# Kernel optimization log

Hardware: AMD Instinct MI355X
Metric: run time of the kernel (lower is better)

Reference implementation:

```python
import jax, jax.numpy as jnp
import numpy as np

# Coefficients expressing each of the 16 soft binary logic gates as
# c0 + ca*a + cb*b + cab*(a*b), in standard difflogic op order:
# 0:False 1:AND 2:a&~b 3:A 4:~a&b 5:B 6:XOR 7:OR 8:NOR 9:XNOR
# 10:~B 11:B=>A 12:~A 13:A=>B 14:NAND 15:True
GATE_COEF = jnp.array([
    [0, 0, 0, 0],
    [0, 0, 0, 1],
    [0, 1, 0, -1],
    [0, 1, 0, 0],
    [0, 0, 1, -1],
    [0, 0, 1, 0],
    [0, 1, 1, -2],
    [0, 1, 1, -1],
    [1, -1, -1, 1],
    [1, -1, -1, 2],
    [1, 0, -1, 0],
    [1, 0, -1, 1],
    [1, -1, 0, 0],
    [1, -1, 0, 1],
    [1, 0, 0, -1],
    [1, 0, 0, 0],
], dtype=jnp.float32)  # [16, 4]

INPUT_DIM = 8192
HIDDEN_DIMS = [16384, 16384, 16384, 16384]
OUTPUT_DIM = 1000
BATCH = 2048
TAU = 1.0
N_GATES = 16


def setup_inputs() -> dict:
    key = jax.random.key(0)
    kx, key = jax.random.split(key)
    inp = {"x": jax.random.uniform(kx, (BATCH, INPUT_DIM), dtype=jnp.float32)}
    dims = [INPUT_DIM] + HIDDEN_DIMS + [OUTPUT_DIM]
    for i in range(len(dims) - 1):
        in_d, out_d = dims[i], dims[i + 1]
        kw, ka, kb, key = jax.random.split(key, 4)
        inp[f"w{i}"] = jax.random.normal(kw, (out_d, N_GATES), dtype=jnp.float32)
        inp[f"ia{i}"] = jax.random.randint(ka, (out_d,), 0, in_d, dtype=jnp.int32)
        inp[f"ib{i}"] = jax.random.randint(kb, (out_d,), 0, in_d, dtype=jnp.int32)
    return inp


def _logic_layer(x, w, ia, ib):
    # gather the two inputs of every neuron: [batch, out_dim]
    a = x[:, ia]
    b = x[:, ib]
    p = jax.nn.softmax(w, axis=-1)              # [out_dim, 16]
    coef = p @ GATE_COEF                         # [out_dim, 4]
    # weighted mixture of all 16 gates, fused via bilinear form
    return coef[:, 0] + coef[:, 1] * a + coef[:, 2] * b + coef[:, 3] * (a * b)


def reference(x, w0, w1, w2, w3, w4, ia0, ia1, ia2, ia3, ia4, ib0, ib1, ib2, ib3, ib4):
    ws = [w0, w1, w2, w3, w4]
    ias = [ia0, ia1, ia2, ia3, ia4]
    ibs = [ib0, ib1, ib2, ib3, ib4]
    h = x
    for w, ia, ib in zip(ws, ias, ibs):
        h = _logic_layer(h, w, ia, ib)
    # GroupSum(output_dim, tau): split last dim into output_dim groups, sum, /tau
    batch = h.shape[0]
    group = h.shape[-1] // OUTPUT_DIM
    out = h.reshape(batch, OUTPUT_DIM, group).sum(-1) / TAU
    return out
```

## Files before the change

kernel.cpp:

```cpp
#include <hip/hip_runtime.h>


#define NBATCH 2048
#define IN_DIM 8192
#define HID 16384
#define OUT_DIM 1000
#define NTOT (4 * HID + OUT_DIM)

typedef __attribute__((ext_vector_type(4))) _Float16 half4;

__device__ __constant__ float GC_dev[64] = {
    0, 0, 0, 0,   0, 0, 0, 1,   0, 1, 0, -1,  0, 1, 0, 0,
    0, 0, 1, -1,  0, 0, 1, 0,   0, 1, 1, -2,  0, 1, 1, -1,
    1, -1, -1, 1, 1, -1, -1, 2, 1, 0, -1, 0,  1, 0, -1, 1,
    1, -1, 0, 0,  1, -1, 0, 1,  1, 0, 0, -1,  1, 0, 0, 0
};

struct PrepArgs {
    const float* w[5];
    const int* ia[5];
    const int* ib[5];
};

__global__ __launch_bounds__(256) void prep_kernel(
    PrepArgs args, half4* __restrict__ coefT, unsigned int* __restrict__ idxT) {
    int g = blockIdx.x * 256 + threadIdx.x;
    if (g >= NTOT) return;
    int l = (g < 4 * HID) ? (g >> 14) : 4;
    int j = g - l * HID;

    const float* wrow = args.w[l] + (size_t)j * 16;
    float v[16];
    const float4* w4 = (const float4*)wrow;
#pragma unroll
    for (int i = 0; i < 4; ++i) {
        float4 t = w4[i];
        v[4 * i + 0] = t.x; v[4 * i + 1] = t.y; v[4 * i + 2] = t.z; v[4 * i + 3] = t.w;
    }
    float m = v[0];
#pragma unroll
    for (int g2 = 1; g2 < 16; ++g2) m = fmaxf(m, v[g2]);
    float s = 0.f;
#pragma unroll
    for (int g2 = 0; g2 < 16; ++g2) { v[g2] = __expf(v[g2] - m); s += v[g2]; }
    float inv = 1.f / s;
    float c0 = 0.f, c1 = 0.f, c2 = 0.f, c3 = 0.f;
#pragma unroll
    for (int g2 = 0; g2 < 16; ++g2) {
        c0 += v[g2] * GC_dev[g2 * 4 + 0];
        c1 += v[g2] * GC_dev[g2 * 4 + 1];
        c2 += v[g2] * GC_dev[g2 * 4 + 2];
        c3 += v[g2] * GC_dev[g2 * 4 + 3];
    }
    half4 c;
    c[0] = (_Float16)(c0 * inv); c[1] = (_Float16)(c1 * inv);
    c[2] = (_Float16)(c2 * inv); c[3] = (_Float16)(c3 * inv);
    coefT[g] = c;
    idxT[g] = (unsigned int)args.ia[l][j] | ((unsigned int)args.ib[l][j] << 16);
}

__global__ __launch_bounds__(512) void fused_kernel(
    const float* __restrict__ x, const half4* __restrict__ coefT,
    const unsigned int* __restrict__ idxT, float* __restrict__ out) {
    __shared__ _Float16 lds[2 * HID];
    int b = blockIdx.x;
    int t = threadIdx.x;

    const float4* xr = (const float4*)(x + (size_t)b * IN_DIM);
#pragma unroll
    for (int i = 0; i < 4; ++i) {
        int j = i * 2048 + t * 4;
        float4 v = xr[i * 512 + t];
        half4 h;
        h[0] = (_Float16)v.x; h[1] = (_Float16)v.y;
        h[2] = (_Float16)v.z; h[3] = (_Float16)v.w;
        *(half4*)&lds[j] = h;
    }
    __syncthreads();

    int inBase = 0, outBase = HID;
    int tabOfs = 0;
#pragma unroll
    for (int l = 0; l < 4; ++l) {
#pragma unroll 4
        for (int j = t; j < HID; j += 512) {
            unsigned int idx = idxT[tabOfs + j];
            half4 c = coefT[tabOfs + j];
            float a = (float)lds[inBase + (idx & 0xFFFFu)];
            float bb = (float)lds[inBase + (idx >> 16)];
            float r = fmaf((float)c[3], a * bb,
                      fmaf((float)c[2], bb,
                      fmaf((float)c[1], a, (float)c[0])));
            lds[outBase + j] = (_Float16)r;
        }
        tabOfs += HID;
        int tmp = inBase; inBase = outBase; outBase = tmp;
        __syncthreads();
    }

    for (int j = t; j < OUT_DIM; j += 512) {
        unsigned int idx = idxT[tabOfs + j];
        half4 c = coefT[tabOfs + j];
        float a = (float)lds[idx & 0xFFFFu];
        float bb = (float)lds[idx >> 16];
        float r = fmaf((float)c[3], a * bb,
                  fmaf((float)c[2], bb,
                  fmaf((float)c[1], a, (float)c[0])));
        out[(size_t)b * OUT_DIM + j] = r;
    }
}

extern "C" void kernel_launch(void* const* d_in, const int* in_sizes, int n_in,
                              void* d_out, int out_size, void* d_ws, size_t ws_size,
                              hipStream_t stream) {
    const float* x = (const float*)d_in[0];
    PrepArgs args;
    for (int i = 0; i < 5; ++i) {
        args.w[i]  = (const float*)d_in[1 + 3 * i];
        args.ia[i] = (const int*)d_in[2 + 3 * i];
        args.ib[i] = (const int*)d_in[3 + 3 * i];
    }

    char* ws = (char*)d_ws;
    half4* coefT = (half4*)ws;
    size_t coefBytes = ((size_t)NTOT * 8 + 255) & ~(size_t)255;
    unsigned int* idxT = (unsigned int*)(ws + coefBytes);

    prep_kernel<<<(NTOT + 255) / 256, 256, 0, stream>>>(args, coefT, idxT);
    fused_kernel<<<NBATCH, 512, 0, stream>>>(x, coefT, idxT, (float*)d_out);
}
```

Before: 205.7 us.

## Process two batch rows per block with interleaved half2 LDS activations

Each block now handles two batch rows, storing their activations interleaved as half2 pairs in LDS, so every gather index and coefficient load serves two samples. Blocks double to 1024 threads and use 128KB of dynamic shared memory. The intent is to halve the global index/coefficient traffic and the LDS gather instruction count per sample. In exchange, occupancy per CU drops because of the doubled LDS footprint, and there are half as many blocks.

```diff
diff --git a/kernel.cpp b/kernel.cpp
--- a/kernel.cpp
+++ b/kernel.cpp
@@ -8,6 +8,7 @@
 #define NTOT (4 * HID + OUT_DIM)
 
 typedef __attribute__((ext_vector_type(4))) _Float16 half4;
+typedef __attribute__((ext_vector_type(2))) _Float16 half2v;
 
 __device__ __constant__ float GC_dev[64] = {
     0, 0, 0, 0,   0, 0, 0, 1,   0, 1, 0, -1,  0, 1, 0, 0,
@@ -59,54 +60,70 @@
     idxT[g] = (unsigned int)args.ia[l][j] | ((unsigned int)args.ib[l][j] << 16);
 }
 
-__global__ __launch_bounds__(512) void fused_kernel(
+__global__ __launch_bounds__(1024) void fused_kernel(
     const float* __restrict__ x, const half4* __restrict__ coefT,
     const unsigned int* __restrict__ idxT, float* __restrict__ out) {
-    __shared__ _Float16 lds[2 * HID];
-    int b = blockIdx.x;
+    extern __shared__ half2v lds[];
+    int bp = blockIdx.x;
     int t = threadIdx.x;
+    int b0 = 2 * bp, b1 = 2 * bp + 1;
 
-    const float4* xr = (const float4*)(x + (size_t)b * IN_DIM);
+    const float4* xr0 = (const float4*)(x + (size_t)b0 * IN_DIM);
+    const float4* xr1 = (const float4*)(x + (size_t)b1 * IN_DIM);
 #pragma unroll
-    for (int i = 0; i < 4; ++i) {
-        int j = i * 2048 + t * 4;
-        float4 v = xr[i * 512 + t];
-        half4 h;
-        h[0] = (_Float16)v.x; h[1] = (_Float16)v.y;
-        h[2] = (_Float16)v.z; h[3] = (_Float16)v.w;
-        *(half4*)&lds[j] = h;
+    for (int i = 0; i < 2; ++i) {
+        int e = i * 1024 + t;
+        float4 v0 = xr0[e];
+        float4 v1 = xr1[e];
+        half2v h0 = {(_Float16)v0.x, (_Float16)v1.x};
+        half2v h1 = {(_Float16)v0.y, (_Float16)v1.y};
+        half2v h2 = {(_Float16)v0.z, (_Float16)v1.z};
+        half2v h3 = {(_Float16)v0.w, (_Float16)v1.w};
+        lds[4 * e + 0] = h0;
+        lds[4 * e + 1] = h1;
+        lds[4 * e + 2] = h2;
+        lds[4 * e + 3] = h3;
     }
     __syncthreads();
 
-    int inBase = 0, outBase = HID;
-    int tabOfs = 0;
+    int inW = 0, outW = HID;
+    int tab = 0;
 #pragma unroll
     for (int l = 0; l < 4; ++l) {
 #pragma unroll 4
-        for (int j = t; j < HID; j += 512) {
-            unsigned int idx = idxT[tabOfs + j];
-            half4 c = coefT[tabOfs + j];
-            float a = (float)lds[inBase + (idx & 0xFFFFu)];
-            float bb = (float)lds[inBase + (idx >> 16)];
-            float r = fmaf((float)c[3], a * bb,
-                      fmaf((float)c[2], bb,
-                      fmaf((float)c[1], a, (float)c[0])));
-            lds[outBase + j] = (_Float16)r;
+        for (int k = 0; k < HID / 1024; ++k) {
+            int j = k * 1024 + t;
+            unsigned int idx = idxT[tab + j];
+            half4 c = coefT[tab + j];
+            half2v ap = lds[inW + (idx & 0xFFFFu)];
+            half2v bq = lds[inW + (idx >> 16)];
+            float c0 = (float)c[0], c1 = (float)c[1];
+            float c2 = (float)c[2], c3 = (float)c[3];
+            float a0 = (float)ap[0], a1 = (float)ap[1];
+            float q0 = (float)bq[0], q1 = (float)bq[1];
+            float r0 = fmaf(c3, a0 * q0, fmaf(c2, q0, fmaf(c1, a0, c0)));
+            float r1 = fmaf(c3, a1 * q1, fmaf(c2, q1, fmaf(c1, a1, c0)));
+            half2v o = {(_Float16)r0, (_Float16)r1};
+            lds[outW + j] = o;
         }
-        tabOfs += HID;
-        int tmp = inBase; inBase = outBase; outBase = tmp;
+        tab += HID;
+        int tmp = inW; inW = outW; outW = tmp;
         __syncthreads();
     }
 
-    for (int j = t; j < OUT_DIM; j += 512) {
-        unsigned int idx = idxT[tabOfs + j];
-        half4 c = coefT[tabOfs + j];
-        float a = (float)lds[idx & 0xFFFFu];
-        float bb = (float)lds[idx >> 16];
-        float r = fmaf((float)c[3], a * bb,
-                  fmaf((float)c[2], bb,
-                  fmaf((float)c[1], a, (float)c[0])));
-        out[(size_t)b * OUT_DIM + j] = r;
+    if (t < OUT_DIM) {
+        unsigned int idx = idxT[tab + t];
+        half4 c = coefT[tab + t];
+        half2v ap = lds[idx & 0xFFFFu];
+        half2v bq = lds[idx >> 16];
+        float c0 = (float)c[0], c1 = (float)c[1];
+        float c2 = (float)c[2], c3 = (float)c[3];
+        float a0 = (float)ap[0], a1 = (float)ap[1];
+        float q0 = (float)bq[0], q1 = (float)bq[1];
+        out[(size_t)b0 * OUT_DIM + t] =
+            fmaf(c3, a0 * q0, fmaf(c2, q0, fmaf(c1, a0, c0)));
+        out[(size_t)b1 * OUT_DIM + t] =
+            fmaf(c3, a1 * q1, fmaf(c2, q1, fmaf(c1, a1, c0)));
     }
 }
 
@@ -127,5 +144,6 @@
     unsigned int* idxT = (unsigned int*)(ws + coefBytes);
 
     prep_kernel<<<(NTOT + 255) / 256, 256, 0, stream>>>(args, coefT, idxT);
-    fused_kernel<<<NBATCH, 512, 0, stream>>>(x, coefT, idxT, (float*)d_out);
+    fused_kernel<<<NBATCH / 2, 1024, 2 * HID * sizeof(half2v), stream>>>(
+        x, coefT, idxT, (float*)d_out);
 }
```

After: 175.6 us. 1.17x faster.
